# Optimization experiments

Measured on AMD Instinct MI355X. Metric: run time of the kernel, lower is better.

The kernel has to match this reference:

```python
import jax, jax.numpy as jnp
import numpy as np

# tinygemm asymmetric int4 convention
QUANT_MIN, QUANT_MAX = 0, 15
MID_POINT = (QUANT_MAX + QUANT_MIN + 1) / 2.0  # 8.0
OUT_F, IN_F, GROUP = 8192, 8192, 128
M_TOKENS = 64


def setup_inputs() -> dict:
    key = jax.random.key(0)
    kx, kw = jax.random.split(key)
    x = jax.random.normal(kx, (M_TOKENS, IN_F), dtype=jnp.float32)
    # Materialize quantized params exactly as quantize_weight_tinygemm does.
    w = jax.random.normal(kw, (OUT_F, IN_F), dtype=jnp.float32) * 0.02
    ng = IN_F // GROUP
    wg = w.reshape(OUT_F, ng, GROUP)
    min_val = wg.min(axis=2)
    max_val = wg.max(axis=2)
    scale = jnp.maximum((max_val - min_val) / float(QUANT_MAX - QUANT_MIN), 1.1920929e-7)
    zero_point = min_val + scale * MID_POINT
    min_val_recon = zero_point - scale * MID_POINT
    q = jnp.clip(jnp.round((wg - min_val_recon[..., None]) / scale[..., None]),
                 QUANT_MIN, QUANT_MAX).astype(jnp.int32)
    int_data = q.reshape(OUT_F, IN_F)  # values in [0, 15]
    # tinygemm layout: (n_groups, out_features, 2) with [..., 0]=scale, [..., 1]=zero_point
    scale_and_zero = jnp.stack([scale, zero_point], axis=-1).transpose(1, 0, 2)
    return {"x": x, "int_data": int_data, "scale_and_zero": scale_and_zero}


def reference(x, int_data, scale_and_zero):
    # Dequant: w = (q - MID_POINT) * scale + zero_point, per group of GROUP along in_features.
    ng = IN_F // GROUP
    q = int_data.reshape(OUT_F, ng, GROUP).astype(x.dtype)
    scale = scale_and_zero[..., 0].T[:, :, None]       # (OUT_F, ng, 1)
    zero_point = scale_and_zero[..., 1].T[:, :, None]  # (OUT_F, ng, 1)
    w = ((q - MID_POINT) * scale + zero_point).reshape(OUT_F, IN_F)
    return x @ w.T  # (M, OUT_F)
```

## Files before the change

kernel.cpp:

```cpp
#include <hip/hip_runtime.h>


#define OUT_F 8192
#define IN_F  8192
#define M_TOK 64
#define GROUP 128
#define BN    128
#define KSPLIT 16
#define KR    (IN_F / KSPLIT)
#define PW_DW (IN_F / 8)

typedef short short8 __attribute__((ext_vector_type(8)));
typedef float f32x4  __attribute__((ext_vector_type(4)));
typedef int   int4v  __attribute__((ext_vector_type(4)));

__device__ __forceinline__ int pack_bf2(float lo, float hi) {
    unsigned ul = __float_as_uint(lo) + 0x8000u;
    unsigned uh = __float_as_uint(hi) + 0x8000u;
    return (int)((ul >> 16) | (uh & 0xFFFF0000u));
}

__global__ __launch_bounds__(256)
void woq_pack(const int* __restrict__ qw, unsigned* __restrict__ pw) {
    const int tid = blockIdx.x * 256 + threadIdx.x;
    const int4* p = (const int4*)(qw + (size_t)tid * 8);
    int4 a = p[0];
    int4 b = p[1];
    unsigned w = (unsigned)a.x        | ((unsigned)a.y << 4)
               | ((unsigned)a.z << 8) | ((unsigned)a.w << 12)
               | ((unsigned)b.x << 16)| ((unsigned)b.y << 20)
               | ((unsigned)b.z << 24)| ((unsigned)b.w << 28);
    pw[tid] = w;
}

__global__ __launch_bounds__(256, 4)
void woq_gemm_packed(const float*    __restrict__ x,
                     const unsigned* __restrict__ pw,
                     const float*    __restrict__ sz,
                     float*          __restrict__ outp) {
    __shared__ int lds_x[16 * 64 * 4];

    const int t    = threadIdx.x;
    const int lane = t & 63;
    const int wv   = t >> 6;
    const int n0   = blockIdx.x * BN;
    const int k0   = blockIdx.y * KR;

    const int nlo  = lane & 15;
    const int quad = lane >> 4;

    const int n1 = n0 + wv * 32 + nlo;
    const int n2 = n1 + 16;
    const unsigned* pw1 = pw + (size_t)n1 * PW_DW + quad;
    const unsigned* pw2 = pw + (size_t)n2 * PW_DW + quad;

    f32x4 acc[4][2];
#pragma unroll
    for (int mi = 0; mi < 4; ++mi)
#pragma unroll
        for (int ni = 0; ni < 2; ++ni)
            acc[mi][ni] = (f32x4){0.f, 0.f, 0.f, 0.f};

    for (int g = 0; g < KR / GROUP; ++g) {
        const int kg = k0 + g * GROUP;
        const int gg = kg >> 7;

        const float2 p1 = *(const float2*)(sz + ((size_t)gg * OUT_F + n1) * 2);
        const float2 p2 = *(const float2*)(sz + ((size_t)gg * OUT_F + n2) * 2);
        const float s1 = p1.x, c1 = fmaf(-8.f, p1.x, p1.y);
        const float s2 = p2.x, c2 = fmaf(-8.f, p2.x, p2.y);

        __syncthreads();
#pragma unroll
        for (int i = 0; i < 4; ++i) {
            int slot  = t + 256 * i;
            int chunk = slot >> 6;
            int l     = slot & 63;
            int m     = ((chunk & 3) << 4) + (l & 15);
            int kk    = ((chunk >> 2) << 5) + ((l >> 4) << 3);
            const float4* p = (const float4*)(x + (size_t)m * IN_F + kg + kk);
            float4 v0 = p[0];
            float4 v1 = p[1];
            int4v bv;
            bv.x = pack_bf2(v0.x, v0.y);
            bv.y = pack_bf2(v0.z, v0.w);
            bv.z = pack_bf2(v1.x, v1.y);
            bv.w = pack_bf2(v1.z, v1.w);
            *(int4v*)&lds_x[slot * 4] = bv;
        }
        __syncthreads();

        const int dwg = kg >> 3;

#pragma unroll
        for (int ks = 0; ks < 4; ++ks) {
            const unsigned w1 = pw1[dwg + ks * 4];
            const unsigned w2 = pw2[dwg + ks * 4];

            short8 a[4];
#pragma unroll
            for (int mi = 0; mi < 4; ++mi)
                a[mi] = *(const short8*)&lds_x[((ks * 4 + mi) * 64 + lane) * 4];

            float v1f[8], v2f[8];
#pragma unroll
            for (int j = 0; j < 8; ++j) {
                v1f[j] = fmaf((float)((w1 >> (4 * j)) & 15u), s1, c1);
                v2f[j] = fmaf((float)((w2 >> (4 * j)) & 15u), s2, c2);
            }
            int4v b1i, b2i;
            b1i.x = pack_bf2(v1f[0], v1f[1]);
            b1i.y = pack_bf2(v1f[2], v1f[3]);
            b1i.z = pack_bf2(v1f[4], v1f[5]);
            b1i.w = pack_bf2(v1f[6], v1f[7]);
            b2i.x = pack_bf2(v2f[0], v2f[1]);
            b2i.y = pack_bf2(v2f[2], v2f[3]);
            b2i.z = pack_bf2(v2f[4], v2f[5]);
            b2i.w = pack_bf2(v2f[6], v2f[7]);
            short8 b1 = __builtin_bit_cast(short8, b1i);
            short8 b2 = __builtin_bit_cast(short8, b2i);

#pragma unroll
            for (int mi = 0; mi < 4; ++mi) {
                acc[mi][0] = __builtin_amdgcn_mfma_f32_16x16x32_bf16(a[mi], b1, acc[mi][0], 0, 0, 0);
                acc[mi][1] = __builtin_amdgcn_mfma_f32_16x16x32_bf16(a[mi], b2, acc[mi][1], 0, 0, 0);
            }
        }
    }

    float* dst = outp + (size_t)blockIdx.y * (M_TOK * OUT_F);
#pragma unroll
    for (int mi = 0; mi < 4; ++mi) {
#pragma unroll
        for (int ni = 0; ni < 2; ++ni) {
            const int n = n0 + wv * 32 + ni * 16 + nlo;
#pragma unroll
            for (int r = 0; r < 4; ++r) {
                const int m = mi * 16 + quad * 4 + r;
                dst[(size_t)m * OUT_F + n] = acc[mi][ni][r];
            }
        }
    }
}

__global__ __launch_bounds__(256, 4)
void woq_gemm_atomic(const float* __restrict__ x,
                     const int*   __restrict__ qw,
                     const float* __restrict__ sz,
                     float*       __restrict__ outp) {
    __shared__ int lds_x[16 * 64 * 4];
    const int t = threadIdx.x, lane = t & 63, wv = t >> 6;
    const int n0 = blockIdx.x * BN, k0 = blockIdx.y * KR;
    const int nlo = lane & 15, quad = lane >> 4, kq8 = quad << 3;
    const int n1 = n0 + wv * 32 + nlo, n2 = n1 + 16;
    f32x4 acc[4][2];
#pragma unroll
    for (int mi = 0; mi < 4; ++mi)
#pragma unroll
        for (int ni = 0; ni < 2; ++ni) acc[mi][ni] = (f32x4){0.f, 0.f, 0.f, 0.f};
    for (int g = 0; g < KR / GROUP; ++g) {
        const int kg = k0 + g * GROUP, gg = kg >> 7;
        const float2 p1 = *(const float2*)(sz + ((size_t)gg * OUT_F + n1) * 2);
        const float2 p2 = *(const float2*)(sz + ((size_t)gg * OUT_F + n2) * 2);
        const float s1 = p1.x, c1 = fmaf(-8.f, p1.x, p1.y);
        const float s2 = p2.x, c2 = fmaf(-8.f, p2.x, p2.y);
        __syncthreads();
#pragma unroll
        for (int i = 0; i < 4; ++i) {
            int slot = t + 256 * i, chunk = slot >> 6, l = slot & 63;
            int m = ((chunk & 3) << 4) + (l & 15);
            int kk = ((chunk >> 2) << 5) + ((l >> 4) << 3);
            const float4* p = (const float4*)(x + (size_t)m * IN_F + kg + kk);
            float4 v0 = p[0], v1 = p[1];
            int4v bv;
            bv.x = pack_bf2(v0.x, v0.y); bv.y = pack_bf2(v0.z, v0.w);
            bv.z = pack_bf2(v1.x, v1.y); bv.w = pack_bf2(v1.z, v1.w);
            *(int4v*)&lds_x[slot * 4] = bv;
        }
        __syncthreads();
#pragma unroll
        for (int ks = 0; ks < 4; ++ks) {
            const int k = kg + ks * 32;
            const int* q1p = qw + (size_t)n1 * IN_F + k + kq8;
            const int* q2p = qw + (size_t)n2 * IN_F + k + kq8;
            const int4 qa = *(const int4*)(q1p), qb = *(const int4*)(q1p + 4);
            const int4 qc = *(const int4*)(q2p), qd = *(const int4*)(q2p + 4);
            short8 a[4];
#pragma unroll
            for (int mi = 0; mi < 4; ++mi)
                a[mi] = *(const short8*)&lds_x[((ks * 4 + mi) * 64 + lane) * 4];
            int4v b1i, b2i;
            b1i.x = pack_bf2(fmaf((float)qa.x, s1, c1), fmaf((float)qa.y, s1, c1));
            b1i.y = pack_bf2(fmaf((float)qa.z, s1, c1), fmaf((float)qa.w, s1, c1));
            b1i.z = pack_bf2(fmaf((float)qb.x, s1, c1), fmaf((float)qb.y, s1, c1));
            b1i.w = pack_bf2(fmaf((float)qb.z, s1, c1), fmaf((float)qb.w, s1, c1));
            b2i.x = pack_bf2(fmaf((float)qc.x, s2, c2), fmaf((float)qc.y, s2, c2));
            b2i.y = pack_bf2(fmaf((float)qc.z, s2, c2), fmaf((float)qc.w, s2, c2));
            b2i.z = pack_bf2(fmaf((float)qd.x, s2, c2), fmaf((float)qd.y, s2, c2));
            b2i.w = pack_bf2(fmaf((float)qd.z, s2, c2), fmaf((float)qd.w, s2, c2));
            short8 b1 = __builtin_bit_cast(short8, b1i);
            short8 b2 = __builtin_bit_cast(short8, b2i);
#pragma unroll
            for (int mi = 0; mi < 4; ++mi) {
                acc[mi][0] = __builtin_amdgcn_mfma_f32_16x16x32_bf16(a[mi], b1, acc[mi][0], 0, 0, 0);
                acc[mi][1] = __builtin_amdgcn_mfma_f32_16x16x32_bf16(a[mi], b2, acc[mi][1], 0, 0, 0);
            }
        }
    }
#pragma unroll
    for (int mi = 0; mi < 4; ++mi)
#pragma unroll
        for (int ni = 0; ni < 2; ++ni) {
            const int n = n0 + wv * 32 + ni * 16 + nlo;
#pragma unroll
            for (int r = 0; r < 4; ++r) {
                const int m = mi * 16 + quad * 4 + r;
                atomicAdd(outp + (size_t)m * OUT_F + n, acc[mi][ni][r]);
            }
        }
}

__global__ __launch_bounds__(256)
void woq_reduce(const float* __restrict__ part, float* __restrict__ out) {
    const int i = (blockIdx.x * 256 + threadIdx.x) * 4;
    const size_t stride = (size_t)M_TOK * OUT_F;
    float4 s = *(const float4*)(part + i);
#pragma unroll
    for (int k = 1; k < KSPLIT; ++k) {
        float4 v = *(const float4*)(part + (size_t)k * stride + i);
        s.x += v.x; s.y += v.y; s.z += v.z; s.w += v.w;
    }
    *(float4*)(out + i) = s;
}

extern "C" void kernel_launch(void* const* d_in, const int* in_sizes, int n_in,
                              void* d_out, int out_size, void* d_ws, size_t ws_size,
                              hipStream_t stream) {
    const float* x  = (const float*)d_in[0];
    const int*   qw = (const int*)d_in[1];
    const float* sz = (const float*)d_in[2];
    float* out = (float*)d_out;

    const size_t pw_bytes   = (size_t)OUT_F * PW_DW * sizeof(unsigned);
    const size_t part_bytes = (size_t)KSPLIT * M_TOK * OUT_F * sizeof(float);
    dim3 grid(OUT_F / BN, KSPLIT);

    if (ws_size >= pw_bytes + part_bytes) {
        unsigned* pw  = (unsigned*)d_ws;
        float*    part = (float*)((char*)d_ws + pw_bytes);
        woq_pack<<<(OUT_F * PW_DW) / 256, 256, 0, stream>>>(qw, pw);
        woq_gemm_packed<<<grid, 256, 0, stream>>>(x, pw, sz, part);
        woq_reduce<<<(M_TOK * OUT_F) / (256 * 4), 256, 0, stream>>>(part, out);
    } else {
        hipMemsetAsync(d_out, 0, (size_t)out_size * sizeof(float), stream);
        woq_gemm_atomic<<<grid, 256, 0, stream>>>(x, qw, sz, out);
    }
}
```

Measured before the change: 403.8 us.

## Fuse int4 weight packing into GEMM via swizzled LDS staging and halve split-K

Removes the separate packing kernel and the packed-weight round trip. The GEMM now loads the raw int32 quantized weights directly into a swizzled shared-memory tile per group and dequantizes from there. Split-K drops from 16 to 8, which shrinks the partial-sum buffer and reduce work. In exchange each block needs much more LDS and registers, lowering occupancy to 2 blocks per CU, and the GEMM itself reads 8x more weight bytes.

```diff
diff --git a/kernel.cpp b/kernel.cpp
--- a/kernel.cpp
+++ b/kernel.cpp
@@ -6,9 +6,8 @@
 #define M_TOK 64
 #define GROUP 128
 #define BN    128
-#define KSPLIT 16
+#define KSPLIT 8
 #define KR    (IN_F / KSPLIT)
-#define PW_DW (IN_F / 8)
 
 typedef short short8 __attribute__((ext_vector_type(8)));
 typedef float f32x4  __attribute__((ext_vector_type(4)));
@@ -20,24 +19,12 @@
     return (int)((ul >> 16) | (uh & 0xFFFF0000u));
 }
 
-__global__ __launch_bounds__(256)
-void woq_pack(const int* __restrict__ qw, unsigned* __restrict__ pw) {
-    const int tid = blockIdx.x * 256 + threadIdx.x;
-    const int4* p = (const int4*)(qw + (size_t)tid * 8);
-    int4 a = p[0];
-    int4 b = p[1];
-    unsigned w = (unsigned)a.x        | ((unsigned)a.y << 4)
-               | ((unsigned)a.z << 8) | ((unsigned)a.w << 12)
-               | ((unsigned)b.x << 16)| ((unsigned)b.y << 20)
-               | ((unsigned)b.z << 24)| ((unsigned)b.w << 28);
-    pw[tid] = w;
-}
-
-__global__ __launch_bounds__(256, 4)
-void woq_gemm_packed(const float*    __restrict__ x,
-                     const unsigned* __restrict__ pw,
-                     const float*    __restrict__ sz,
-                     float*          __restrict__ outp) {
+__global__ __launch_bounds__(256, 2)
+void woq_gemm(const float* __restrict__ x,
+              const int*   __restrict__ qw,
+              const float* __restrict__ sz,
+              float*       __restrict__ part) {
+    __shared__ int qtile[128 * 128];
     __shared__ int lds_x[16 * 64 * 4];
 
     const int t    = threadIdx.x;
@@ -48,11 +35,15 @@
 
     const int nlo  = lane & 15;
     const int quad = lane >> 4;
-
-    const int n1 = n0 + wv * 32 + nlo;
-    const int n2 = n1 + 16;
-    const unsigned* pw1 = pw + (size_t)n1 * PW_DW + quad;
-    const unsigned* pw2 = pw + (size_t)n2 * PW_DW + quad;
+    const int swz  = nlo & 7;
+
+    const int r1 = wv * 32 + nlo;
+    const int r2 = r1 + 16;
+    const int n1 = n0 + r1;
+    const int n2 = n0 + r2;
+
+    const int st_row = t >> 5;
+    const int st_kb  = t & 31;
 
     f32x4 acc[4][2];
 #pragma unroll
@@ -71,6 +62,20 @@
         const float s2 = p2.x, c2 = fmaf(-8.f, p2.x, p2.y);
 
         __syncthreads();
+
+        int4 qbuf[16];
+#pragma unroll
+        for (int i = 0; i < 16; ++i) {
+            const int row = st_row + i * 8;
+            qbuf[i] = *(const int4*)(qw + (size_t)(n0 + row) * IN_F + kg + st_kb * 4);
+        }
+#pragma unroll
+        for (int i = 0; i < 16; ++i) {
+            const int row = st_row + i * 8;
+            const int kbp = st_kb ^ (row & 7);
+            *(int4v*)&qtile[row * 128 + kbp * 4] = (int4v){qbuf[i].x, qbuf[i].y, qbuf[i].z, qbuf[i].w};
+        }
+
 #pragma unroll
         for (int i = 0; i < 4; ++i) {
             int slot  = t + 256 * i;
@@ -90,33 +95,29 @@
         }
         __syncthreads();
 
-        const int dwg = kg >> 3;
-
 #pragma unroll
         for (int ks = 0; ks < 4; ++ks) {
-            const unsigned w1 = pw1[dwg + ks * 4];
-            const unsigned w2 = pw2[dwg + ks * 4];
+            const int kb0 = ks * 8 + quad * 2;
+
+            const int4v qa = *(const int4v*)&qtile[r1 * 128 + ((kb0     ^ swz) << 2)];
+            const int4v qb = *(const int4v*)&qtile[r1 * 128 + (((kb0+1) ^ swz) << 2)];
+            const int4v qc = *(const int4v*)&qtile[r2 * 128 + ((kb0     ^ swz) << 2)];
+            const int4v qd = *(const int4v*)&qtile[r2 * 128 + (((kb0+1) ^ swz) << 2)];
 
             short8 a[4];
 #pragma unroll
             for (int mi = 0; mi < 4; ++mi)
                 a[mi] = *(const short8*)&lds_x[((ks * 4 + mi) * 64 + lane) * 4];
 
-            float v1f[8], v2f[8];
-#pragma unroll
-            for (int j = 0; j < 8; ++j) {
-                v1f[j] = fmaf((float)((w1 >> (4 * j)) & 15u), s1, c1);
-                v2f[j] = fmaf((float)((w2 >> (4 * j)) & 15u), s2, c2);
-            }
             int4v b1i, b2i;
-            b1i.x = pack_bf2(v1f[0], v1f[1]);
-            b1i.y = pack_bf2(v1f[2], v1f[3]);
-            b1i.z = pack_bf2(v1f[4], v1f[5]);
-            b1i.w = pack_bf2(v1f[6], v1f[7]);
-            b2i.x = pack_bf2(v2f[0], v2f[1]);
-            b2i.y = pack_bf2(v2f[2], v2f[3]);
-            b2i.z = pack_bf2(v2f[4], v2f[5]);
-            b2i.w = pack_bf2(v2f[6], v2f[7]);
+            b1i.x = pack_bf2(fmaf((float)qa.x, s1, c1), fmaf((float)qa.y, s1, c1));
+            b1i.y = pack_bf2(fmaf((float)qa.z, s1, c1), fmaf((float)qa.w, s1, c1));
+            b1i.z = pack_bf2(fmaf((float)qb.x, s1, c1), fmaf((float)qb.y, s1, c1));
+            b1i.w = pack_bf2(fmaf((float)qb.z, s1, c1), fmaf((float)qb.w, s1, c1));
+            b2i.x = pack_bf2(fmaf((float)qc.x, s2, c2), fmaf((float)qc.y, s2, c2));
+            b2i.y = pack_bf2(fmaf((float)qc.z, s2, c2), fmaf((float)qc.w, s2, c2));
+            b2i.z = pack_bf2(fmaf((float)qd.x, s2, c2), fmaf((float)qd.y, s2, c2));
+            b2i.w = pack_bf2(fmaf((float)qd.z, s2, c2), fmaf((float)qd.w, s2, c2));
             short8 b1 = __builtin_bit_cast(short8, b1i);
             short8 b2 = __builtin_bit_cast(short8, b2i);
 
@@ -128,7 +129,7 @@
         }
     }
 
-    float* dst = outp + (size_t)blockIdx.y * (M_TOK * OUT_F);
+    float* dst = part + (size_t)blockIdx.y * (M_TOK * OUT_F);
 #pragma unroll
     for (int mi = 0; mi < 4; ++mi) {
 #pragma unroll
@@ -141,6 +142,19 @@
             }
         }
     }
+}
+
+__global__ __launch_bounds__(256)
+void woq_reduce(const float* __restrict__ part, float* __restrict__ out) {
+    const int i = (blockIdx.x * 256 + threadIdx.x) * 4;
+    const size_t stride = (size_t)M_TOK * OUT_F;
+    float4 s = *(const float4*)(part + i);
+#pragma unroll
+    for (int k = 1; k < KSPLIT; ++k) {
+        float4 v = *(const float4*)(part + (size_t)k * stride + i);
+        s.x += v.x; s.y += v.y; s.z += v.z; s.w += v.w;
+    }
+    *(float4*)(out + i) = s;
 }
 
 __global__ __launch_bounds__(256, 4)
@@ -220,19 +234,6 @@
         }
 }
 
-__global__ __launch_bounds__(256)
-void woq_reduce(const float* __restrict__ part, float* __restrict__ out) {
-    const int i = (blockIdx.x * 256 + threadIdx.x) * 4;
-    const size_t stride = (size_t)M_TOK * OUT_F;
-    float4 s = *(const float4*)(part + i);
-#pragma unroll
-    for (int k = 1; k < KSPLIT; ++k) {
-        float4 v = *(const float4*)(part + (size_t)k * stride + i);
-        s.x += v.x; s.y += v.y; s.z += v.z; s.w += v.w;
-    }
-    *(float4*)(out + i) = s;
-}
-
 extern "C" void kernel_launch(void* const* d_in, const int* in_sizes, int n_in,
                               void* d_out, int out_size, void* d_ws, size_t ws_size,
                               hipStream_t stream) {
@@ -241,15 +242,12 @@
     const float* sz = (const float*)d_in[2];
     float* out = (float*)d_out;
 
-    const size_t pw_bytes   = (size_t)OUT_F * PW_DW * sizeof(unsigned);
     const size_t part_bytes = (size_t)KSPLIT * M_TOK * OUT_F * sizeof(float);
     dim3 grid(OUT_F / BN, KSPLIT);
 
-    if (ws_size >= pw_bytes + part_bytes) {
-        unsigned* pw  = (unsigned*)d_ws;
-        float*    part = (float*)((char*)d_ws + pw_bytes);
-        woq_pack<<<(OUT_F * PW_DW) / 256, 256, 0, stream>>>(qw, pw);
-        woq_gemm_packed<<<grid, 256, 0, stream>>>(x, pw, sz, part);
+    if (ws_size >= part_bytes) {
+        float* part = (float*)d_ws;
+        woq_gemm<<<grid, 256, 0, stream>>>(x, qw, sz, part);
         woq_reduce<<<(M_TOK * OUT_F) / (256 * 4), 256, 0, stream>>>(part, out);
     } else {
         hipMemsetAsync(d_out, 0, (size_t)out_size * sizeof(float), stream);
```

New measurement: 396.8 us. Within noise of the previous version (-1.8%).
